# Optimization experiments

Hardware: AMD Instinct MI355X
Metric: run time of the kernel (lower is better)

The kernel has to match this reference:

```python
import jax, jax.numpy as jnp
import numpy as np

B, L, D, H = 2, 2048, 1024, 16
HD = D // H  # head_dim = 64


def setup_inputs() -> dict:
    key = jax.random.key(0)
    ks = jax.random.split(key, 5)
    x = jax.random.normal(ks[0], (B, L, D), dtype=jnp.float32)
    # causal mask: True means masked (as in masked_fill)
    mask = jnp.triu(jnp.ones((L, L), dtype=bool), k=1)[None, None, :, :]
    W_qkv = jax.random.normal(ks[1], (3 * D, D), dtype=jnp.float32) * (1.0 / np.sqrt(D))
    b_qkv = jax.random.normal(ks[2], (3 * D,), dtype=jnp.float32) * 0.02
    W_out = jax.random.normal(ks[3], (D, D), dtype=jnp.float32) * (1.0 / np.sqrt(D))
    b_out = jax.random.normal(ks[4], (D,), dtype=jnp.float32) * 0.02
    return {"x": x, "mask": mask, "W_qkv": W_qkv, "b_qkv": b_qkv,
            "W_out": W_out, "b_out": b_out}


def reference(x, mask, W_qkv, b_qkv, W_out, b_out):
    b, l, d = x.shape
    qkv = x @ W_qkv.T + b_qkv                       # (b, l, 3d)
    q, k, v = jnp.split(qkv, 3, axis=-1)
    # (b, l, d) -> (b, h, l, hd)
    to_heads = lambda t: t.reshape(b, l, H, HD).transpose(0, 2, 1, 3)
    q, k, v = to_heads(q), to_heads(k), to_heads(v)
    scale = 1.0 / jnp.sqrt(jnp.float32(HD))
    a = jnp.einsum('bhqd,bhkd->bhqk', q, k) * scale  # (b, h, l, l)
    a = jnp.where(mask, -jnp.inf, a)
    a = jax.nn.softmax(a, axis=-1)
    out = jnp.einsum('bhqk,bhkd->bhqd', a, v)        # (b, h, l, hd)
    out = out.transpose(0, 2, 1, 3).reshape(b, l, d)
    out = out @ W_out.T + b_out
    return out
```

## Files before the change

### kernel.cpp

```cpp
#include <hip/hip_runtime.h>
#include <hip/hip_bf16.h>

#define LOG2E 1.44269504088896340736f

typedef __attribute__((ext_vector_type(8))) short short8_t;
typedef __attribute__((ext_vector_type(4))) float f32x4_t;
typedef __attribute__((ext_vector_type(4))) unsigned short us4_t;

__device__ __forceinline__ unsigned short f2bf(float f) {
  unsigned u = __builtin_bit_cast(unsigned, f);
  return (unsigned short)((u + 0x7fffu + ((u >> 16) & 1u)) >> 16);
}

__device__ __forceinline__ void gload_lds16(const unsigned short* g, unsigned short* l) {
  __builtin_amdgcn_global_load_lds(
      (const __attribute__((address_space(1))) void*)(g),
      (__attribute__((address_space(3))) void*)(l), 16, 0, 0);
}

__global__ __launch_bounds__(256) void cvt3(
    const float* __restrict__ x, const float* __restrict__ wq, const float* __restrict__ wo,
    unsigned short* __restrict__ xb, unsigned short* __restrict__ wqb,
    unsigned short* __restrict__ wob)
{
  const int n1 = 4096 * 1024 / 4, n2 = 3072 * 1024 / 4, n3 = 1024 * 1024 / 4;
  const int total = n1 + n2 + n3;
  for (int t = blockIdx.x * blockDim.x + threadIdx.x; t < total; t += gridDim.x * blockDim.x) {
    const float* s; unsigned short* d; int off;
    if (t < n1)            { s = x;  d = xb;  off = t * 4; }
    else if (t < n1 + n2)  { s = wq; d = wqb; off = (t - n1) * 4; }
    else                   { s = wo; d = wob; off = (t - n1 - n2) * 4; }
    f32x4_t v = *(const f32x4_t*)(s + off);
    us4_t o = { f2bf(v[0]), f2bf(v[1]), f2bf(v[2]), f2bf(v[3]) };
    *(us4_t*)(d + off) = o;
  }
}

__global__ __launch_bounds__(256) void gemm_qkv(
    const unsigned short* __restrict__ A, const unsigned short* __restrict__ Bw,
    const float* __restrict__ bias,
    unsigned short* __restrict__ Qp, unsigned short* __restrict__ Kp,
    unsigned short* __restrict__ Vtp, int M, int N, int K)
{
  __shared__ alignas(16) unsigned short lA[128 * 32];
  __shared__ alignas(16) unsigned short lB[128 * 32];
  const int tid = threadIdx.x, lane = tid & 63, w = tid >> 6;
  const int lo = lane & 15, hi = lane >> 4;
  const int bm = blockIdx.y * 128, bn = blockIdx.x * 128;
  const int wm = (w >> 1) * 64, wn = (w & 1) * 64;

  const f32x4_t zero = {0.f, 0.f, 0.f, 0.f};
  f32x4_t acc[4][4];
#pragma unroll
  for (int i = 0; i < 4; ++i)
#pragma unroll
    for (int j = 0; j < 4; ++j) acc[i][j] = zero;

  const unsigned short* gA[2]; const unsigned short* gB[2];
  unsigned short* lAp[2]; unsigned short* lBp[2];
#pragma unroll
  for (int i = 0; i < 2; ++i) {
    int offb = (i * 4 + w) * 1024;
    int off  = offb + lane * 16;
    int row  = off >> 6;
    int ke   = (off & 63) >> 1;
    gA[i]  = &A [(size_t)(bm + row) * K + ke];
    gB[i]  = &Bw[(size_t)(bn + row) * K + ke];
    lAp[i] = &lA[offb >> 1];
    lBp[i] = &lB[offb >> 1];
  }

  for (int k0 = 0; k0 < K; k0 += 32) {
#pragma unroll
    for (int i = 0; i < 2; ++i) {
      gload_lds16(gA[i] + k0, lAp[i]);
      gload_lds16(gB[i] + k0, lBp[i]);
    }
    __syncthreads();
    short8_t af[4], bb[4];
#pragma unroll
    for (int i = 0; i < 4; ++i) af[i] = *(const short8_t*)&lA[(wm + i * 16 + lo) * 32 + hi * 8];
#pragma unroll
    for (int j = 0; j < 4; ++j) bb[j] = *(const short8_t*)&lB[(wn + j * 16 + lo) * 32 + hi * 8];
#pragma unroll
    for (int i = 0; i < 4; ++i)
#pragma unroll
      for (int j = 0; j < 4; ++j)
        acc[i][j] = __builtin_amdgcn_mfma_f32_16x16x32_bf16(af[i], bb[j], acc[i][j], 0, 0, 0);
    __syncthreads();
  }

#pragma unroll
  for (int i = 0; i < 4; ++i) {
#pragma unroll
    for (int j = 0; j < 4; ++j) {
      int col = bn + wn + j * 16 + lo;
      float bv = bias[col];
#pragma unroll
      for (int r = 0; r < 4; ++r) {
        int row = bm + wm + i * 16 + hi * 4 + r;
        float v = acc[i][j][r] + bv;
        unsigned short hv = f2bf(v);
        int sec = col >> 10, h = (col >> 6) & 15, d = col & 63;
        int b = row >> 11, ll = row & 2047;
        int bh = b * 16 + h;
        if (sec == 0)      Qp [((size_t)bh * 2048 + ll) * 64 + d] = hv;
        else if (sec == 1) Kp [((size_t)bh * 2048 + ll) * 64 + d] = hv;
        else               Vtp[((size_t)bh * 64 + d) * 2048 + ll] = hv;
      }
    }
  }
}

__global__ __launch_bounds__(256) void gemm_out(
    const unsigned short* __restrict__ A, const unsigned short* __restrict__ Bw,
    const float* __restrict__ bias, float* __restrict__ Cf, int M, int N, int K)
{
  __shared__ alignas(16) unsigned short lA[64 * 32];
  __shared__ alignas(16) unsigned short lB[64 * 32];
  const int tid = threadIdx.x, lane = tid & 63, w = tid >> 6;
  const int lo = lane & 15, hi = lane >> 4;
  const int bm = blockIdx.y * 64, bn = blockIdx.x * 64;

  const f32x4_t zero = {0.f, 0.f, 0.f, 0.f};
  f32x4_t acc[4] = {zero, zero, zero, zero};

  const int off = w * 1024 + lane * 16;
  const int row = off >> 6, ke = (off & 63) >> 1;
  const unsigned short* gA = &A [(size_t)(bm + row) * K + ke];
  const unsigned short* gB = &Bw[(size_t)(bn + row) * K + ke];
  unsigned short* lAp = &lA[(w * 1024) >> 1];
  unsigned short* lBp = &lB[(w * 1024) >> 1];

  for (int k0 = 0; k0 < K; k0 += 32) {
    gload_lds16(gA + k0, lAp);
    gload_lds16(gB + k0, lBp);
    __syncthreads();
    short8_t af = *(const short8_t*)&lA[(w * 16 + lo) * 32 + hi * 8];
    short8_t bb[4];
#pragma unroll
    for (int j = 0; j < 4; ++j) bb[j] = *(const short8_t*)&lB[(j * 16 + lo) * 32 + hi * 8];
#pragma unroll
    for (int j = 0; j < 4; ++j)
      acc[j] = __builtin_amdgcn_mfma_f32_16x16x32_bf16(af, bb[j], acc[j], 0, 0, 0);
    __syncthreads();
  }

#pragma unroll
  for (int j = 0; j < 4; ++j) {
    int col = bn + j * 16 + lo;
    float bv = bias[col];
#pragma unroll
    for (int r = 0; r < 4; ++r) {
      int row2 = bm + w * 16 + hi * 4 + r;
      Cf[(size_t)row2 * N + col] = acc[j][r] + bv;
    }
  }
}

__global__ __launch_bounds__(256) void attn(
    const unsigned short* __restrict__ Q, const unsigned short* __restrict__ K,
    const unsigned short* __restrict__ V, unsigned short* __restrict__ AO)
{
  const int tid = threadIdx.x, lane = tid & 63, w = tid >> 6;
  const int lo = lane & 15, hi = lane >> 4;
  const int qt = 31 - blockIdx.y;
  const int bh = blockIdx.x;
  const int qbase = qt * 64 + w * 16;
  const int nt = qt + 1;
  const unsigned short* Qb = Q + (size_t)bh * 2048 * 64;
  const unsigned short* Kb = K + (size_t)bh * 2048 * 64;
  const unsigned short* Vb = V + (size_t)bh * 64 * 2048;

  __shared__ alignas(16) unsigned short lK[2][8 * 512];
  __shared__ alignas(16) unsigned short lV[2][8 * 512];
  __shared__ alignas(16) unsigned short pl[4][16 * 72];
  unsigned short* myP = &pl[w][0];

  short8_t qf0 = *(const short8_t*)&Qb[(qbase + lo) * 64 + hi * 8];
  short8_t qf1 = *(const short8_t*)&Qb[(qbase + lo) * 64 + 32 + hi * 8];

  const f32x4_t zero = {0.f, 0.f, 0.f, 0.f};
  f32x4_t o[4] = {zero, zero, zero, zero};
  float m[4] = {-INFINITY, -INFINITY, -INFINITY, -INFINITY};
  float l[4] = {0.f, 0.f, 0.f, 0.f};
  const float SC = 0.125f * LOG2E;
  const float THR = 8.0f;

  const unsigned short* ksrc = Kb + (size_t)lane * 64 + 2 * w * 8;
  const unsigned short* vsrc = Vb + (size_t)lane * 2048 + 2 * w * 8;
  unsigned short* kd0 = &lK[0][2 * w * 512];
  unsigned short* kd1 = &lK[1][2 * w * 512];
  unsigned short* vd0 = &lV[0][2 * w * 512];
  unsigned short* vd1 = &lV[1][2 * w * 512];

  gload_lds16(ksrc,     kd0);
  gload_lds16(ksrc + 8, kd0 + 512);
  gload_lds16(vsrc,     vd0);
  gload_lds16(vsrc + 8, vd0 + 512);

  for (int t = 0; t < nt; ++t) {
    const int kb = t * 64;
    const int cur = t & 1;
    __syncthreads();

    if (t + 1 < nt) {
      const unsigned short* ks = ksrc + (size_t)(kb + 64) * 64;
      const unsigned short* vs = vsrc + (kb + 64);
      unsigned short* kd = cur ? kd0 : kd1;
      unsigned short* vd = cur ? vd0 : vd1;
      gload_lds16(ks,     kd);
      gload_lds16(ks + 8, kd + 512);
      gload_lds16(vs,     vd);
      gload_lds16(vs + 8, vd + 512);
    }
    const unsigned short* lk = cur ? &lK[1][0] : &lK[0][0];
    const unsigned short* lv = cur ? &lV[1][0] : &lV[0][0];

    f32x4_t s4[4] = {zero, zero, zero, zero};
    __builtin_amdgcn_s_setprio(1);
#pragma unroll
    for (int s = 0; s < 4; ++s) {
      short8_t k0 = *(const short8_t*)&lk[(hi * 64 + s * 16 + lo) * 8];
      short8_t k1 = *(const short8_t*)&lk[((4 + hi) * 64 + s * 16 + lo) * 8];
      s4[s] = __builtin_amdgcn_mfma_f32_16x16x32_bf16(qf0, k0, s4[s], 0, 0, 0);
      s4[s] = __builtin_amdgcn_mfma_f32_16x16x32_bf16(qf1, k1, s4[s], 0, 0, 0);
    }
    __builtin_amdgcn_s_setprio(0);

    const bool needmask = (kb + 64 > qbase);
    float a[4][4];
    float pm[4];
#pragma unroll
    for (int r = 0; r < 4; ++r) {
      int q = qbase + hi * 4 + r;
#pragma unroll
      for (int s = 0; s < 4; ++s) {
        float av = s4[s][r] * SC;
        if (needmask && (kb + s * 16 + lo > q)) av = -INFINITY;
        a[r][s] = av;
      }
      pm[r] = fmaxf(fmaxf(a[r][0], a[r][1]), fmaxf(a[r][2], a[r][3]));
    }

    bool ok = (pm[0] - m[0] <= THR) && (pm[1] - m[1] <= THR) &&
              (pm[2] - m[2] <= THR) && (pm[3] - m[3] <= THR);
    if (!__all(ok)) {
#pragma unroll
      for (int r = 0; r < 4; ++r) {
        float t2 = pm[r];
        t2 = fmaxf(t2, __shfl_xor(t2, 1));
        t2 = fmaxf(t2, __shfl_xor(t2, 2));
        t2 = fmaxf(t2, __shfl_xor(t2, 4));
        t2 = fmaxf(t2, __shfl_xor(t2, 8));
        float mn = fmaxf(m[r], t2);
        float f = __builtin_amdgcn_exp2f(m[r] - mn);
        m[r] = mn;
        l[r] *= f;
#pragma unroll
        for (int j = 0; j < 4; ++j) o[j][r] *= f;
      }
    }

#pragma unroll
    for (int r = 0; r < 4; ++r) {
      float e0 = __builtin_amdgcn_exp2f(a[r][0] - m[r]);
      float e1 = __builtin_amdgcn_exp2f(a[r][1] - m[r]);
      float e2 = __builtin_amdgcn_exp2f(a[r][2] - m[r]);
      float e3 = __builtin_amdgcn_exp2f(a[r][3] - m[r]);
      l[r] += (e0 + e1) + (e2 + e3);
      int prow = (hi * 4 + r) * 72;
      myP[prow + lo]      = f2bf(e0);
      myP[prow + 16 + lo] = f2bf(e1);
      myP[prow + 32 + lo] = f2bf(e2);
      myP[prow + 48 + lo] = f2bf(e3);
    }

    short8_t pf0 = *(const short8_t*)&myP[lo * 72 + hi * 8];
    short8_t pf1 = *(const short8_t*)&myP[lo * 72 + 32 + hi * 8];
    __builtin_amdgcn_s_setprio(1);
#pragma unroll
    for (int j = 0; j < 4; ++j) {
      short8_t v0 = *(const short8_t*)&lv[(hi * 64 + j * 16 + lo) * 8];
      short8_t v1 = *(const short8_t*)&lv[((4 + hi) * 64 + j * 16 + lo) * 8];
      o[j] = __builtin_amdgcn_mfma_f32_16x16x32_bf16(pf0, v0, o[j], 0, 0, 0);
      o[j] = __builtin_amdgcn_mfma_f32_16x16x32_bf16(pf1, v1, o[j], 0, 0, 0);
    }
    __builtin_amdgcn_s_setprio(0);
  }

  const int b = bh >> 4, h = bh & 15;
#pragma unroll
  for (int r = 0; r < 4; ++r) {
    float ls = l[r];
    ls += __shfl_xor(ls, 1);
    ls += __shfl_xor(ls, 2);
    ls += __shfl_xor(ls, 4);
    ls += __shfl_xor(ls, 8);
    float inv = 1.0f / ls;
    int qrow = qbase + hi * 4 + r;
    size_t base = ((size_t)b * 2048 + qrow) * 1024 + h * 64;
#pragma unroll
    for (int j = 0; j < 4; ++j)
      AO[base + j * 16 + lo] = f2bf(o[j][r] * inv);
  }
}

extern "C" void kernel_launch(void* const* d_in, const int* in_sizes, int n_in,
                              void* d_out, int out_size, void* d_ws, size_t ws_size,
                              hipStream_t stream)
{
  (void)in_sizes; (void)n_in; (void)out_size; (void)ws_size;
  const float* x    = (const float*)d_in[0];
  const float* Wqkv = (const float*)d_in[2];
  const float* bqkv = (const float*)d_in[3];
  const float* Wout = (const float*)d_in[4];
  const float* bout = (const float*)d_in[5];

  unsigned short* ws  = (unsigned short*)d_ws;
  unsigned short* xb  = ws;
  unsigned short* wqb = xb  + 4096 * 1024;
  unsigned short* wob = wqb + 3072 * 1024;
  unsigned short* Qp  = wob + 1024 * 1024;
  unsigned short* Kp  = Qp  + 32 * 2048 * 64;
  unsigned short* Vtp = Kp  + 32 * 2048 * 64;
  unsigned short* AO  = Vtp + 32 * 2048 * 64;

  cvt3<<<dim3(2048), dim3(256), 0, stream>>>(x, Wqkv, Wout, xb, wqb, wob);
  gemm_qkv<<<dim3(24, 32), dim3(256), 0, stream>>>(
      xb, wqb, bqkv, Qp, Kp, Vtp, 4096, 3072, 1024);
  attn<<<dim3(32, 32), dim3(256), 0, stream>>>(Qp, Kp, Vtp, AO);
  gemm_out<<<dim3(16, 64), dim3(256), 0, stream>>>(
      AO, wob, bout, (float*)d_out, 4096, 1024, 1024);
}
```

Baseline: 226.7 us.

## Triple-buffer LDS tiles with async prefetch in QKV and output GEMMs

Both projection GEMMs now keep three LDS buffers and issue global-to-LDS loads two k-tiles ahead. Explicit vmcnt waits and a single barrier per iteration replace the two __syncthreads per tile. MFMA sections are wrapped in s_setprio. The intent is to overlap global memory latency with matrix math and halve the barrier count, at the cost of three times the LDS per block, which may reduce occupancy.

```diff
diff --git a/kernel.cpp b/kernel.cpp
--- a/kernel.cpp
+++ b/kernel.cpp
@@ -42,8 +42,8 @@
     unsigned short* __restrict__ Qp, unsigned short* __restrict__ Kp,
     unsigned short* __restrict__ Vtp, int M, int N, int K)
 {
-  __shared__ alignas(16) unsigned short lA[128 * 32];
-  __shared__ alignas(16) unsigned short lB[128 * 32];
+  __shared__ alignas(16) unsigned short lA[3][128 * 32];
+  __shared__ alignas(16) unsigned short lB[3][128 * 32];
   const int tid = threadIdx.x, lane = tid & 63, w = tid >> 6;
   const int lo = lane & 15, hi = lane >> 4;
   const int bm = blockIdx.y * 128, bn = blockIdx.x * 128;
@@ -57,38 +57,60 @@
     for (int j = 0; j < 4; ++j) acc[i][j] = zero;
 
   const unsigned short* gA[2]; const unsigned short* gB[2];
-  unsigned short* lAp[2]; unsigned short* lBp[2];
+  int aoff[2];
 #pragma unroll
   for (int i = 0; i < 2; ++i) {
-    int offb = (i * 4 + w) * 1024;
-    int off  = offb + lane * 16;
-    int row  = off >> 6;
-    int ke   = (off & 63) >> 1;
-    gA[i]  = &A [(size_t)(bm + row) * K + ke];
-    gB[i]  = &Bw[(size_t)(bn + row) * K + ke];
-    lAp[i] = &lA[offb >> 1];
-    lBp[i] = &lB[offb >> 1];
-  }
-
-  for (int k0 = 0; k0 < K; k0 += 32) {
-#pragma unroll
-    for (int i = 0; i < 2; ++i) {
-      gload_lds16(gA[i] + k0, lAp[i]);
-      gload_lds16(gB[i] + k0, lBp[i]);
-    }
-    __syncthreads();
+    int r = w + i * 4, rowb = r * 16;
+    int row = rowb + (lane >> 2), kf = (lane & 3) * 8;
+    gA[i] = &A [(size_t)(bm + row) * K + kf];
+    gB[i] = &Bw[(size_t)(bn + row) * K + kf];
+    aoff[i] = rowb * 32;
+  }
+
+  const int NT = K >> 5;
+#define QKV_STAGE(T, BI)                                     \
+  {                                                          \
+    int k0_ = (T) * 32;                                      \
+    _Pragma("unroll")                                        \
+    for (int i = 0; i < 2; ++i) {                            \
+      gload_lds16(gA[i] + k0_, &lA[BI][aoff[i]]);            \
+      gload_lds16(gB[i] + k0_, &lB[BI][aoff[i]]);            \
+    }                                                        \
+  }
+
+  QKV_STAGE(0, 0);
+  QKV_STAGE(1, 1);
+  int cur = 0, stg = 2;
+
+  for (int t = 0; t < NT; ++t) {
+    if (t + 1 < NT) {
+      asm volatile("s_waitcnt vmcnt(4)" ::: "memory");
+    } else {
+      asm volatile("s_waitcnt vmcnt(0)" ::: "memory");
+    }
+    __builtin_amdgcn_s_barrier();
+    if (t + 2 < NT) QKV_STAGE(t + 2, stg);
+    __builtin_amdgcn_sched_barrier(0);
+
+    const unsigned short* la = &lA[cur][0];
+    const unsigned short* lb = &lB[cur][0];
     short8_t af[4], bb[4];
 #pragma unroll
-    for (int i = 0; i < 4; ++i) af[i] = *(const short8_t*)&lA[(wm + i * 16 + lo) * 32 + hi * 8];
-#pragma unroll
-    for (int j = 0; j < 4; ++j) bb[j] = *(const short8_t*)&lB[(wn + j * 16 + lo) * 32 + hi * 8];
+    for (int i = 0; i < 4; ++i) af[i] = *(const short8_t*)&la[(wm + i * 16 + lo) * 32 + hi * 8];
+#pragma unroll
+    for (int j = 0; j < 4; ++j) bb[j] = *(const short8_t*)&lb[(wn + j * 16 + lo) * 32 + hi * 8];
+    __builtin_amdgcn_s_setprio(1);
 #pragma unroll
     for (int i = 0; i < 4; ++i)
 #pragma unroll
       for (int j = 0; j < 4; ++j)
         acc[i][j] = __builtin_amdgcn_mfma_f32_16x16x32_bf16(af[i], bb[j], acc[i][j], 0, 0, 0);
-    __syncthreads();
-  }
+    __builtin_amdgcn_s_setprio(0);
+
+    cur = (cur == 2) ? 0 : cur + 1;
+    stg = (stg == 2) ? 0 : stg + 1;
+  }
+#undef QKV_STAGE
 
 #pragma unroll
   for (int i = 0; i < 4; ++i) {
@@ -116,8 +138,8 @@
     const unsigned short* __restrict__ A, const unsigned short* __restrict__ Bw,
     const float* __restrict__ bias, float* __restrict__ Cf, int M, int N, int K)
 {
-  __shared__ alignas(16) unsigned short lA[64 * 32];
-  __shared__ alignas(16) unsigned short lB[64 * 32];
+  __shared__ alignas(16) unsigned short lA[3][64 * 32];
+  __shared__ alignas(16) unsigned short lB[3][64 * 32];
   const int tid = threadIdx.x, lane = tid & 63, w = tid >> 6;
   const int lo = lane & 15, hi = lane >> 4;
   const int bm = blockIdx.y * 64, bn = blockIdx.x * 64;
@@ -125,26 +147,50 @@
   const f32x4_t zero = {0.f, 0.f, 0.f, 0.f};
   f32x4_t acc[4] = {zero, zero, zero, zero};
 
-  const int off = w * 1024 + lane * 16;
-  const int row = off >> 6, ke = (off & 63) >> 1;
-  const unsigned short* gA = &A [(size_t)(bm + row) * K + ke];
-  const unsigned short* gB = &Bw[(size_t)(bn + row) * K + ke];
-  unsigned short* lAp = &lA[(w * 1024) >> 1];
-  unsigned short* lBp = &lB[(w * 1024) >> 1];
-
-  for (int k0 = 0; k0 < K; k0 += 32) {
-    gload_lds16(gA + k0, lAp);
-    gload_lds16(gB + k0, lBp);
-    __syncthreads();
-    short8_t af = *(const short8_t*)&lA[(w * 16 + lo) * 32 + hi * 8];
+  const int rowb = w * 16;
+  const int row = rowb + (lane >> 2), kf = (lane & 3) * 8;
+  const unsigned short* gA = &A [(size_t)(bm + row) * K + kf];
+  const unsigned short* gB = &Bw[(size_t)(bn + row) * K + kf];
+  const int aoff = rowb * 32;
+
+  const int NT = K >> 5;
+#define OUT_STAGE(T, BI)                          \
+  {                                               \
+    int k0_ = (T) * 32;                           \
+    gload_lds16(gA + k0_, &lA[BI][aoff]);         \
+    gload_lds16(gB + k0_, &lB[BI][aoff]);         \
+  }
+
+  OUT_STAGE(0, 0);
+  OUT_STAGE(1, 1);
+  int cur = 0, stg = 2;
+
+  for (int t = 0; t < NT; ++t) {
+    if (t + 1 < NT) {
+      asm volatile("s_waitcnt vmcnt(2)" ::: "memory");
+    } else {
+      asm volatile("s_waitcnt vmcnt(0)" ::: "memory");
+    }
+    __builtin_amdgcn_s_barrier();
+    if (t + 2 < NT) OUT_STAGE(t + 2, stg);
+    __builtin_amdgcn_sched_barrier(0);
+
+    const unsigned short* la = &lA[cur][0];
+    const unsigned short* lb = &lB[cur][0];
+    short8_t af = *(const short8_t*)&la[(w * 16 + lo) * 32 + hi * 8];
     short8_t bb[4];
 #pragma unroll
-    for (int j = 0; j < 4; ++j) bb[j] = *(const short8_t*)&lB[(j * 16 + lo) * 32 + hi * 8];
+    for (int j = 0; j < 4; ++j) bb[j] = *(const short8_t*)&lb[(j * 16 + lo) * 32 + hi * 8];
+    __builtin_amdgcn_s_setprio(1);
 #pragma unroll
     for (int j = 0; j < 4; ++j)
       acc[j] = __builtin_amdgcn_mfma_f32_16x16x32_bf16(af, bb[j], acc[j], 0, 0, 0);
-    __syncthreads();
-  }
+    __builtin_amdgcn_s_setprio(0);
+
+    cur = (cur == 2) ? 0 : cur + 1;
+    stg = (stg == 2) ? 0 : stg + 1;
+  }
+#undef OUT_STAGE
 
 #pragma unroll
   for (int j = 0; j < 4; ++j) {
```

Result: no change. 223.4 us (-1.4%).
